# Optimization experiments

Measured on AMD Instinct MI355X. Metric: run time of the kernel, lower is better.

Reference implementation:

```python
import jax, jax.numpy as jnp
import numpy as np

BETA = 0.9
THR = 1.0
B, T, F, H = 64, 256, 1024, 512

# snntorch heaviside spike with ATan surrogate gradient (alpha=2.0, snntorch default)
@jax.custom_vjp
def spike_fn(u):
    return (u > 0).astype(u.dtype)

def _spike_fwd(u):
    return spike_fn(u), u

def _spike_bwd(u, g):
    alpha = 2.0
    grad = (alpha / 2.0) / (1.0 + (jnp.pi / 2.0 * alpha * u) ** 2)
    return (g * grad,)

spike_fn.defvjp(_spike_fwd, _spike_bwd)


def setup_inputs() -> dict:
    key = jax.random.key(0)
    ks = jax.random.split(key, 12)
    s = 0.05
    return {
        "f_f": jax.random.normal(ks[0], (B, T, F), dtype=jnp.float32),
        "seq_len": jnp.full((B,), T, dtype=jnp.int64),
        "Wf": jax.random.normal(ks[1], (H, F), dtype=jnp.float32) * s,
        "bf": jnp.zeros((H,), jnp.float32),
        "W1": jax.random.normal(ks[2], (H, H), dtype=jnp.float32) * s,
        "b1": jnp.zeros((H,), jnp.float32),
        "W2": jax.random.normal(ks[3], (H, H), dtype=jnp.float32) * s,
        "b2": jnp.zeros((H,), jnp.float32),
        "Mw1": jax.random.normal(ks[4], (512, H), dtype=jnp.float32) * s,
        "Mb1": jnp.zeros((512,), jnp.float32),
        "Mw2": jax.random.normal(ks[5], (32, 512), dtype=jnp.float32) * s,
        "Mb2": jnp.zeros((32,), jnp.float32),
        "Mw3": jax.random.normal(ks[6], (1, 32), dtype=jnp.float32) * s,
        "Mb3": jnp.zeros((1,), jnp.float32),
    }


def _forward(f_f, Wf, bf, W1, b1, W2, b2, Mw1, Mb1, Mw2, Mb2, Mw3, Mb3):
    h = f_f @ Wf.T + bf            # [B,T,H] fc_f
    x1 = h @ W1.T + b1             # layer-1 linear drive precomputed (state-independent)

    def step(carry, x1_t):
        m1, m2 = carry
        # snntorch Leaky (subtract reset): reset from previous mem's spike
        r1 = spike_fn(m1 - THR)
        m1 = BETA * m1 + x1_t - r1 * THR
        s1 = spike_fn(m1 - THR)
        x2 = s1 @ W2.T + b2        # layer-2 linear on spikes (dropout=identity, eval)
        r2 = spike_fn(m2 - THR)
        m2 = BETA * m2 + x2 - r2 * THR
        s2 = spike_fn(m2 - THR)
        return (m1, m2), s2

    init = (jnp.zeros((B, H), h.dtype), jnp.zeros((B, H), h.dtype))
    _, spk = jax.lax.scan(step, init, jnp.swapaxes(x1, 0, 1))  # [T,B,H]
    spk = jnp.swapaxes(spk, 0, 1)                              # [B,T,H]

    z = jax.nn.relu(spk @ Mw1.T + Mb1)
    z = z @ Mw2.T + Mb2
    logits = jax.nn.sigmoid((z @ Mw3.T + Mb3).squeeze(-1))     # [B,T]

    # filter: top-(seq_len//16 + 1) mean per clip; seq_len == T for all clips
    k = T // 16 + 1
    topv, _ = jax.lax.top_k(logits, k)
    return jnp.mean(topv, axis=-1)                             # [B]


def reference(f_f, seq_len, Wf, bf, W1, b1, W2, b2, Mw1, Mb1, Mw2, Mb2, Mw3, Mb3):
    return _forward(f_f, Wf, bf, W1, b1, W2, b2, Mw1, Mb1, Mw2, Mb2, Mw3, Mb3)
```

## Files before the change

### kernel.cpp

```cpp
#include <hip/hip_runtime.h>
#include <math.h>

#define BETA 0.9f
#define THR 1.0f

constexpr int B_ = 64, T_ = 256, F_ = 1024, H_ = 512;
constexpr int M_ = B_ * T_;

typedef float f32x4 __attribute__((ext_vector_type(4)));
typedef short short8 __attribute__((ext_vector_type(8)));
typedef _Float16 half8 __attribute__((ext_vector_type(8)));
typedef unsigned short us4 __attribute__((ext_vector_type(4)));
typedef unsigned short ushort_t;

static __device__ __forceinline__ unsigned short f2bf(float x) {
    unsigned b = __builtin_bit_cast(unsigned, x);
    unsigned r = (b + 0x7FFFu + ((b >> 16) & 1u)) >> 16;
    return (unsigned short)r;
}
static __device__ __forceinline__ float bf2f(unsigned short u) {
    unsigned v = ((unsigned)u) << 16;
    return __builtin_bit_cast(float, v);
}
static __device__ __forceinline__ unsigned short f2h(float x) {
    _Float16 h = (_Float16)x;
    return __builtin_bit_cast(unsigned short, h);
}
static __device__ __forceinline__ float h2f(unsigned short u) {
    return (float)__builtin_bit_cast(_Float16, u);
}
static __device__ __forceinline__ int swz(int r) {
    return ((r >> 2) & 3) ^ (r & 3);
}

#define GLDS(srcp, dstp)                                                      \
    __builtin_amdgcn_global_load_lds(                                         \
        (const __attribute__((address_space(1))) unsigned int*)(srcp),        \
        (__attribute__((address_space(3))) unsigned int*)(dstp), 16, 0, 0)

__global__ __launch_bounds__(256) void gemm_scan(
    const ushort_t* __restrict__ Ap, const ushort_t* __restrict__ Bp,
    const float* __restrict__ bias, ushort_t* __restrict__ Sout, int K) {
    __shared__ ushort_t lds[20480];

    const int tid = threadIdx.x;
    const int w = tid >> 6, l = tid & 63;
    const int flat = blockIdx.y * gridDim.x + blockIdx.x;
    const int clip = ((flat >> 6) << 3) | (flat & 7);
    const int strip = (flat >> 3) & 7;
    const int n0 = strip * 64;
    const int m0 = clip * 256;

    f32x4 acc[4][4];
#pragma unroll
    for (int mi = 0; mi < 4; ++mi)
#pragma unroll
        for (int ni = 0; ni < 4; ++ni) acc[mi][ni] = (f32x4){0.f, 0.f, 0.f, 0.f};

    const int c0 = l >> 4;
    const int schunk = (l & 7) ^ ((l >> 3) & 7);
    for (int k0 = 0; k0 < K; k0 += 64) {
        __syncthreads();
#pragma unroll
        for (int j = 0; j < 10; ++j) {
            const int seg = w * 10 + j;
            if (seg < 32) {
                const int r = seg * 8 + (l >> 3);
                GLDS(Ap + (size_t)(m0 + r) * K + k0 + schunk * 8,
                     &lds[seg * 512]);
            } else {
                const int r = (seg - 32) * 8 + (l >> 3);
                GLDS(Bp + (size_t)(n0 + r) * K + k0 + schunk * 8,
                     &lds[16384 + (seg - 32) * 512]);
            }
        }
        __syncthreads();

#pragma unroll
        for (int kh = 0; kh < 2; ++kh) {
            half8 aa[4], bb[4];
            const int q = kh * 4 + c0;
#pragma unroll
            for (int mi = 0; mi < 4; ++mi) {
                const int r = w * 64 + mi * 16 + (l & 15);
                const int off = r * 64 + ((q ^ (l & 7)) * 8);
                aa[mi] = __builtin_bit_cast(half8, *(const short8*)&lds[off]);
            }
#pragma unroll
            for (int ni = 0; ni < 4; ++ni) {
                const int r = ni * 16 + (l & 15);
                const int off = 16384 + r * 64 + ((q ^ (l & 7)) * 8);
                bb[ni] = __builtin_bit_cast(half8, *(const short8*)&lds[off]);
            }
#pragma unroll
            for (int mi = 0; mi < 4; ++mi)
#pragma unroll
                for (int ni = 0; ni < 4; ++ni)
                    acc[mi][ni] = __builtin_amdgcn_mfma_f32_16x16x32_f16(
                        aa[mi], bb[ni], acc[mi][ni], 0, 0, 0);
        }
    }

    __syncthreads();

    float bv[4];
#pragma unroll
    for (int ni = 0; ni < 4; ++ni) bv[ni] = bias[n0 + ni * 16 + (l & 15)];
#pragma unroll
    for (int mi = 0; mi < 4; ++mi) {
        const int t0 = w * 64 + mi * 16 + ((l >> 4) << 2);
#pragma unroll
        for (int ni = 0; ni < 4; ++ni) {
            const int h = ni * 16 + (l & 15);
#pragma unroll
            for (int r = 0; r < 4; ++r)
                lds[(t0 + r) * 66 + h] = f2h(acc[mi][ni][r] + bv[ni]);
        }
    }
    __syncthreads();

    if (tid < 64) {
        const int h = tid;
        ushort_t* sp = Sout + (size_t)m0 * 512 + n0 + h;
        float m = 0.f;
#pragma unroll 4
        for (int t = 0; t < T_; ++t) {
            const float xv = h2f(lds[t * 66 + h]);
            const float r = (m - THR > 0.f) ? THR : 0.f;
            m = BETA * m + xv - r;
            sp[(size_t)t * 512] = (m - THR > 0.f) ? (ushort_t)0x3C00 : (ushort_t)0;
        }
    }
}

__global__ __launch_bounds__(256) void gemm_mil(
    const ushort_t* __restrict__ Ap, const ushort_t* __restrict__ Bp,
    const float* __restrict__ bias, const float* __restrict__ Uv,
    float* __restrict__ part, int N, int K) {
    __shared__ ushort_t lds[16384];

    const int tid = threadIdx.x;
    const int w = tid >> 6, l = tid & 63;
    const int flat = blockIdx.y * gridDim.x + blockIdx.x;
    const int mt = ((flat >> 5) << 3) | (flat & 7);
    const int st = (flat >> 3) & 3;
    const int n0 = st * 128;
    const int m0 = mt * 128;
    const int wr = w >> 1, wc = w & 1;

    f32x4 acc[4][4];
#pragma unroll
    for (int mi = 0; mi < 4; ++mi)
#pragma unroll
        for (int ni = 0; ni < 4; ++ni) acc[mi][ni] = (f32x4){0.f, 0.f, 0.f, 0.f};

    const int c0 = l >> 4;
    const int schunk = (l & 7) ^ ((l >> 3) & 7);
    for (int k0 = 0; k0 < K; k0 += 64) {
        __syncthreads();
#pragma unroll
        for (int j = 0; j < 8; ++j) {
            const int g = w * 8 + j;
            const int seg = g & 15;
            const int r = seg * 8 + (l >> 3);
            const ushort_t* pl = (g < 16) ? Ap : Bp;
            const int rb = (g < 16) ? m0 : n0;
            GLDS(pl + (size_t)(rb + r) * K + k0 + schunk * 8, &lds[g * 512]);
        }
        __syncthreads();

#pragma unroll
        for (int kh = 0; kh < 2; ++kh) {
            half8 aa[4], bb[4];
            const int q = kh * 4 + c0;
#pragma unroll
            for (int mi = 0; mi < 4; ++mi) {
                const int r = wr * 64 + mi * 16 + (l & 15);
                const int off = r * 64 + ((q ^ (l & 7)) * 8);
                aa[mi] = __builtin_bit_cast(half8, *(const short8*)&lds[off]);
            }
#pragma unroll
            for (int ni = 0; ni < 4; ++ni) {
                const int r = wc * 64 + ni * 16 + (l & 15);
                const int off = 8192 + r * 64 + ((q ^ (l & 7)) * 8);
                bb[ni] = __builtin_bit_cast(half8, *(const short8*)&lds[off]);
            }
#pragma unroll
            for (int mi = 0; mi < 4; ++mi)
#pragma unroll
                for (int ni = 0; ni < 4; ++ni)
                    acc[mi][ni] = __builtin_amdgcn_mfma_f32_16x16x32_f16(
                        aa[mi], bb[ni], acc[mi][ni], 0, 0, 0);
        }
    }

    float bv[4], uc[4];
#pragma unroll
    for (int ni = 0; ni < 4; ++ni) {
        const int col = n0 + wc * 64 + ni * 16 + (l & 15);
        bv[ni] = bias[col];
        uc[ni] = Uv[col];
    }
    const int strip = (n0 >> 6) + wc;
#pragma unroll
    for (int mi = 0; mi < 4; ++mi) {
        float p[4];
#pragma unroll
        for (int r = 0; r < 4; ++r) {
            float s = 0.f;
#pragma unroll
            for (int ni = 0; ni < 4; ++ni)
                s += fmaxf(acc[mi][ni][r] + bv[ni], 0.f) * uc[ni];
            p[r] = s;
        }
#pragma unroll
        for (int off = 1; off <= 8; off <<= 1)
#pragma unroll
            for (int r = 0; r < 4; ++r) p[r] += __shfl_xor(p[r], off);
        if ((l & 15) == 0) {
            const int row0 = m0 + wr * 64 + mi * 16 + ((l >> 4) << 2);
#pragma unroll
            for (int r = 0; r < 4; ++r)
                part[(size_t)strip * M_ + row0 + r] = p[r];
        }
    }
}

__global__ __launch_bounds__(256) void gemm_bf16_wc(
    const ushort_t* __restrict__ Ah, const ushort_t* __restrict__ Al,
    const ushort_t* __restrict__ Bh, const ushort_t* __restrict__ Bl,
    ushort_t* __restrict__ Cout, int N, int K) {
    __shared__ ushort_t lds[4 * 4096];

    const int tid = threadIdx.x;
    const int w = tid >> 6, l = tid & 63;
    const int nwg = gridDim.x * gridDim.y;
    const int flat = blockIdx.y * gridDim.x + blockIdx.x;
    const int wg = (flat & 7) * (nwg >> 3) + (flat >> 3);
    const int n0 = (wg % gridDim.x) * 128;
    const int m0 = (wg / gridDim.x) * 128;
    const int wr = w >> 1, wc = w & 1;

    f32x4 acc[4][4];
#pragma unroll
    for (int mi = 0; mi < 4; ++mi)
#pragma unroll
        for (int ni = 0; ni < 4; ++ni) acc[mi][ni] = (f32x4){0.f, 0.f, 0.f, 0.f};

    const int c0 = l >> 4;
    for (int k0 = 0; k0 < K; k0 += 32) {
        __syncthreads();
#pragma unroll
        for (int j = 0; j < 8; ++j) {
            const int g = w * 8 + j;
            const int p = g >> 3, seg = g & 7;
            const int r = seg * 16 + (l >> 2);
            const int ch = (l & 3) ^ swz(r);
            const ushort_t* pl = (p == 0) ? Ah : (p == 1) ? Al : (p == 2) ? Bh : Bl;
            const int rb = (p < 2) ? m0 : n0;
            GLDS(pl + (size_t)(rb + r) * K + k0 + ch * 8,
                 &lds[p * 4096 + seg * 512]);
        }
        __syncthreads();

        short8 ah[4], al[4], bh[4], bl[4];
#pragma unroll
        for (int mi = 0; mi < 4; ++mi) {
            const int r = wr * 64 + mi * 16 + (l & 15);
            const int off = r * 32 + ((c0 ^ swz(r)) * 8);
            ah[mi] = *(const short8*)&lds[off];
            al[mi] = *(const short8*)&lds[4096 + off];
        }
#pragma unroll
        for (int ni = 0; ni < 4; ++ni) {
            const int r = wc * 64 + ni * 16 + (l & 15);
            const int off = r * 32 + ((c0 ^ swz(r)) * 8);
            bh[ni] = *(const short8*)&lds[8192 + off];
            bl[ni] = *(const short8*)&lds[12288 + off];
        }
#pragma unroll
        for (int mi = 0; mi < 4; ++mi)
#pragma unroll
            for (int ni = 0; ni < 4; ++ni) {
                acc[mi][ni] = __builtin_amdgcn_mfma_f32_16x16x32_bf16(
                    ah[mi], bh[ni], acc[mi][ni], 0, 0, 0);
                acc[mi][ni] = __builtin_amdgcn_mfma_f32_16x16x32_bf16(
                    ah[mi], bl[ni], acc[mi][ni], 0, 0, 0);
                acc[mi][ni] = __builtin_amdgcn_mfma_f32_16x16x32_bf16(
                    al[mi], bh[ni], acc[mi][ni], 0, 0, 0);
            }
    }

#pragma unroll
    for (int ni = 0; ni < 4; ++ni) {
        const int col = n0 + wc * 64 + ni * 16 + (l & 15);
#pragma unroll
        for (int mi = 0; mi < 4; ++mi) {
            const int row0 = m0 + wr * 64 + mi * 16 + ((l >> 4) << 2);
#pragma unroll
            for (int r = 0; r < 4; ++r)
                Cout[(size_t)(row0 + r) * N + col] = f2h(acc[mi][ni][r]);
        }
    }
}

__global__ __launch_bounds__(256) void prep_small(
    const float* __restrict__ W1, const float* __restrict__ W2,
    const float* __restrict__ Mw1, const float* __restrict__ bfv,
    const float* __restrict__ b1, const float* __restrict__ Mw2,
    const float* __restrict__ Mb2, const float* __restrict__ Mw3,
    const float* __restrict__ Mb3, const float* __restrict__ Wf,
    ushort_t* __restrict__ w1h, ushort_t* __restrict__ w1l,
    ushort_t* __restrict__ w2f, ushort_t* __restrict__ m1f,
    float* __restrict__ bc, float* __restrict__ uc,
    ushort_t* __restrict__ wfTh, ushort_t* __restrict__ wfTl) {
    __shared__ float tile[32][33];
    const int blk = blockIdx.x;
    const int tid = threadIdx.x;
    if (blk < 256) {
        const int i = blk * 256 + tid;
        f32x4 v = ((const f32x4*)W1)[i];
        us4 h, ll;
#pragma unroll
        for (int e = 0; e < 4; ++e) {
            const unsigned short hb = f2bf(v[e]);
            h[e] = hb;
            ll[e] = f2bf(v[e] - bf2f(hb));
        }
        ((us4*)w1h)[i] = h;
        ((us4*)w1l)[i] = ll;
    } else if (blk < 512) {
        const int i = (blk - 256) * 256 + tid;
        f32x4 v = ((const f32x4*)W2)[i];
        us4 h;
#pragma unroll
        for (int e = 0; e < 4; ++e) h[e] = f2h(v[e]);
        ((us4*)w2f)[i] = h;
    } else if (blk < 768) {
        const int i = (blk - 512) * 256 + tid;
        f32x4 v = ((const f32x4*)Mw1)[i];
        us4 h;
#pragma unroll
        for (int e = 0; e < 4; ++e) h[e] = f2h(v[e]);
        ((us4*)m1f)[i] = h;
    } else if (blk < 896) {
        const int w = tid >> 6, l = tid & 63;
        const int j = (blk - 768) * 4 + w;
        const float* row = W1 + (size_t)j * 512;
        float a = 0.f;
#pragma unroll
        for (int i = 0; i < 8; ++i) a += row[l + i * 64] * bfv[l + i * 64];
#pragma unroll
        for (int off = 32; off >= 1; off >>= 1) a += __shfl_xor(a, off);
        if (l == 0) bc[j] = a + b1[j];
    } else if (blk < 898) {
        const int j = (blk - 896) * 256 + tid;
        float a = 0.f;
        for (int i = 0; i < 32; ++i) a += Mw3[i] * Mw2[(size_t)i * 512 + j];
        uc[j] = a;
        if (j == 0) {
            float c = Mb3[0];
            for (int i = 0; i < 32; ++i) c += Mw3[i] * Mb2[i];
            uc[512] = c;
        }
    } else {
        const int idx = blk - 898;
        const int k0 = (idx & 31) * 32;
        const int i0 = (idx >> 5) * 32;
        const int tx = tid & 31;
        const int ty = tid >> 5;
#pragma unroll
        for (int e = 0; e < 4; ++e) {
            const int i = ty + e * 8;
            tile[i][tx] = Wf[(size_t)(i0 + i) * 1024 + k0 + tx];
        }
        __syncthreads();
#pragma unroll
        for (int e = 0; e < 4; ++e) {
            const int kk = ty + e * 8;
            const float v = tile[tx][kk];
            const unsigned short h = f2bf(v);
            wfTh[(size_t)(k0 + kk) * 512 + i0 + tx] = h;
            wfTl[(size_t)(k0 + kk) * 512 + i0 + tx] = f2bf(v - bf2f(h));
        }
    }
}

__global__ __launch_bounds__(256) void round_f16(const float* __restrict__ x,
                                                 ushort_t* __restrict__ o,
                                                 int n4) {
    int i = blockIdx.x * 256 + threadIdx.x;
    const int stride = gridDim.x * 256;
    for (; i < n4; i += stride) {
        f32x4 v = ((const f32x4*)x)[i];
        us4 h;
#pragma unroll
        for (int e = 0; e < 4; ++e) h[e] = f2h(v[e]);
        ((us4*)o)[i] = h;
    }
}

__global__ __launch_bounds__(64) void tail_topk(const float* __restrict__ part,
                                                const float* __restrict__ uc,
                                                float* __restrict__ out) {
    const int b = blockIdx.x;
    const int lane = threadIdx.x;
    const float c = uc[512];
    float v[4];
#pragma unroll
    for (int i = 0; i < 4; ++i) {
        const int row = b * T_ + lane + i * 64;
        float a = 0.f;
#pragma unroll
        for (int s = 0; s < 8; ++s) a += part[(size_t)s * M_ + row];
        v[i] = a + c;
    }
    float sum = 0.f;
    for (int iter = 0; iter < 17; ++iter) {
        float mv = v[0];
        int mslot = 0;
#pragma unroll
        for (int i = 1; i < 4; ++i)
            if (v[i] > mv) { mv = v[i]; mslot = i; }
        float bv = mv;
        int bl = lane, bs = mslot;
#pragma unroll
        for (int off = 32; off >= 1; off >>= 1) {
            const float ov = __shfl_xor(bv, off);
            const int ol = __shfl_xor(bl, off);
            const int os = __shfl_xor(bs, off);
            if (ov > bv || (ov == bv && ol < bl)) { bv = ov; bl = ol; bs = os; }
        }
        sum += 1.f / (1.f + expf(-bv));
        if (lane == bl) v[bs] = -1e30f;
    }
    if (lane == 0) out[b] = sum * (1.f / 17.f);
}

extern "C" void kernel_launch(void* const* d_in, const int* in_sizes, int n_in,
                              void* d_out, int out_size, void* d_ws, size_t ws_size,
                              hipStream_t stream) {
    const float* f_f = (const float*)d_in[0];
    const float* Wf  = (const float*)d_in[2];
    const float* bf  = (const float*)d_in[3];
    const float* W1  = (const float*)d_in[4];
    const float* b1  = (const float*)d_in[5];
    const float* W2  = (const float*)d_in[6];
    const float* b2  = (const float*)d_in[7];
    const float* Mw1 = (const float*)d_in[8];
    const float* Mb1 = (const float*)d_in[9];
    const float* Mw2 = (const float*)d_in[10];
    const float* Mb2 = (const float*)d_in[11];
    const float* Mw3 = (const float*)d_in[12];
    const float* Mb3 = (const float*)d_in[13];
    float* out = (float*)d_out;

    char* ws = (char*)d_ws;
    const size_t NEf = (size_t)M_ * F_;
    const size_t NE = (size_t)M_ * H_;
    ushort_t* ffh = (ushort_t*)ws;
    ushort_t* sbuf1 = ffh + NEf;
    ushort_t* sbuf2 = sbuf1 + NE;
    ushort_t* w1h = sbuf2 + NE;
    ushort_t* w1l = w1h + 262144;
    ushort_t* w2f = w1l + 262144;
    ushort_t* m1f = w2f + 262144;
    ushort_t* wfTh = m1f + 262144;
    ushort_t* wfTl = wfTh + 524288;
    ushort_t* wcf = wfTl + 524288;
    float* bc = (float*)(wcf + 524288);
    float* uc = bc + 512;
    float* part = uc + 513 + 63;

    const dim3 blk(256);

    prep_small<<<dim3(1410), blk, 0, stream>>>(W1, W2, Mw1, bf, b1, Mw2, Mb2,
                                               Mw3, Mb3, Wf, w1h, w1l, w2f,
                                               m1f, bc, uc, wfTh, wfTl);
    round_f16<<<dim3(2048), blk, 0, stream>>>(f_f, ffh, 4194304);

    gemm_bf16_wc<<<dim3(8, 4), blk, 0, stream>>>(w1h, w1l, wfTh, wfTl, wcf,
                                                 1024, 512);
    gemm_scan<<<dim3(8, 64), blk, 0, stream>>>(ffh, wcf, bc, sbuf1, 1024);
    gemm_scan<<<dim3(8, 64), blk, 0, stream>>>(sbuf1, w2f, b2, sbuf2, 512);
    gemm_mil<<<dim3(4, 128), blk, 0, stream>>>(sbuf2, m1f, Mb1, uc, part,
                                               512, 512);
    tail_topk<<<dim3(B_), dim3(64), 0, stream>>>(part, uc, out);
}
```

Baseline: 124.9 us.

## Double-buffer LDS in scan and MIL GEMMs; fold f16 rounding into prep kernel

The gemm_scan and gemm_mil kernels now keep two LDS buffers and issue the global-to-LDS loads for the next K tile before computing on the current one. This uses one barrier per iteration where there were two, and is meant to overlap memory latency with MFMA work. The standalone round_f16 launch is merged into prep_small as extra blocks, which saves one kernel launch. The cost is double the LDS per block (80KB for gemm_scan), which may lower occupancy. Correctness also relies on the single barrier per tile ordering the async load_lds writes against reads of the other buffer.

Measured after the change: 119.7 us. 1.04x faster.

```diff
diff --git a/kernel.cpp b/kernel.cpp
--- a/kernel.cpp
+++ b/kernel.cpp
@@ -41,7 +41,8 @@
 __global__ __launch_bounds__(256) void gemm_scan(
     const ushort_t* __restrict__ Ap, const ushort_t* __restrict__ Bp,
     const float* __restrict__ bias, ushort_t* __restrict__ Sout, int K) {
-    __shared__ ushort_t lds[20480];
+    constexpr int BUF = 20480;
+    __shared__ ushort_t lds[2 * BUF];
 
     const int tid = threadIdx.x;
     const int w = tid >> 6, l = tid & 63;
@@ -59,22 +60,30 @@
 
     const int c0 = l >> 4;
     const int schunk = (l & 7) ^ ((l >> 3) & 7);
-    for (int k0 = 0; k0 < K; k0 += 64) {
-        __syncthreads();
+
+    auto stage = [&](int buf, int k0) {
 #pragma unroll
         for (int j = 0; j < 10; ++j) {
             const int seg = w * 10 + j;
             if (seg < 32) {
                 const int r = seg * 8 + (l >> 3);
                 GLDS(Ap + (size_t)(m0 + r) * K + k0 + schunk * 8,
-                     &lds[seg * 512]);
+                     &lds[buf + seg * 512]);
             } else {
                 const int r = (seg - 32) * 8 + (l >> 3);
                 GLDS(Bp + (size_t)(n0 + r) * K + k0 + schunk * 8,
-                     &lds[16384 + (seg - 32) * 512]);
+                     &lds[buf + 16384 + (seg - 32) * 512]);
             }
         }
+    };
+
+    const int nt = K / 64;
+    stage(0, 0);
+    for (int t = 0; t < nt; ++t) {
+        const int cur = (t & 1) * BUF;
+        const int nxt = BUF - cur;
         __syncthreads();
+        if (t + 1 < nt) stage(nxt, (t + 1) * 64);
 
 #pragma unroll
         for (int kh = 0; kh < 2; ++kh) {
@@ -83,13 +92,13 @@
 #pragma unroll
             for (int mi = 0; mi < 4; ++mi) {
                 const int r = w * 64 + mi * 16 + (l & 15);
-                const int off = r * 64 + ((q ^ (l & 7)) * 8);
+                const int off = cur + r * 64 + ((q ^ (l & 7)) * 8);
                 aa[mi] = __builtin_bit_cast(half8, *(const short8*)&lds[off]);
             }
 #pragma unroll
             for (int ni = 0; ni < 4; ++ni) {
                 const int r = ni * 16 + (l & 15);
-                const int off = 16384 + r * 64 + ((q ^ (l & 7)) * 8);
+                const int off = cur + 16384 + r * 64 + ((q ^ (l & 7)) * 8);
                 bb[ni] = __builtin_bit_cast(half8, *(const short8*)&lds[off]);
             }
 #pragma unroll
@@ -100,8 +109,6 @@
                         aa[mi], bb[ni], acc[mi][ni], 0, 0, 0);
         }
     }
-
-    __syncthreads();
 
     float bv[4];
 #pragma unroll
@@ -137,7 +144,8 @@
     const ushort_t* __restrict__ Ap, const ushort_t* __restrict__ Bp,
     const float* __restrict__ bias, const float* __restrict__ Uv,
     float* __restrict__ part, int N, int K) {
-    __shared__ ushort_t lds[16384];
+    constexpr int BUF = 16384;
+    __shared__ ushort_t lds[2 * BUF];
 
     const int tid = threadIdx.x;
     const int w = tid >> 6, l = tid & 63;
@@ -156,8 +164,8 @@
 
     const int c0 = l >> 4;
     const int schunk = (l & 7) ^ ((l >> 3) & 7);
-    for (int k0 = 0; k0 < K; k0 += 64) {
-        __syncthreads();
+
+    auto stage = [&](int buf, int k0) {
 #pragma unroll
         for (int j = 0; j < 8; ++j) {
             const int g = w * 8 + j;
@@ -165,9 +173,18 @@
             const int r = seg * 8 + (l >> 3);
             const ushort_t* pl = (g < 16) ? Ap : Bp;
             const int rb = (g < 16) ? m0 : n0;
-            GLDS(pl + (size_t)(rb + r) * K + k0 + schunk * 8, &lds[g * 512]);
-        }
+            GLDS(pl + (size_t)(rb + r) * K + k0 + schunk * 8,
+                 &lds[buf + g * 512]);
+        }
+    };
+
+    const int nt = K / 64;
+    stage(0, 0);
+    for (int t = 0; t < nt; ++t) {
+        const int cur = (t & 1) * BUF;
+        const int nxt = BUF - cur;
         __syncthreads();
+        if (t + 1 < nt) stage(nxt, (t + 1) * 64);
 
 #pragma unroll
         for (int kh = 0; kh < 2; ++kh) {
@@ -176,13 +193,13 @@
 #pragma unroll
             for (int mi = 0; mi < 4; ++mi) {
                 const int r = wr * 64 + mi * 16 + (l & 15);
-                const int off = r * 64 + ((q ^ (l & 7)) * 8);
+                const int off = cur + r * 64 + ((q ^ (l & 7)) * 8);
                 aa[mi] = __builtin_bit_cast(half8, *(const short8*)&lds[off]);
             }
 #pragma unroll
             for (int ni = 0; ni < 4; ++ni) {
                 const int r = wc * 64 + ni * 16 + (l & 15);
-                const int off = 8192 + r * 64 + ((q ^ (l & 7)) * 8);
+                const int off = cur + 8192 + r * 64 + ((q ^ (l & 7)) * 8);
                 bb[ni] = __builtin_bit_cast(half8, *(const short8*)&lds[off]);
             }
 #pragma unroll
@@ -310,10 +327,11 @@
     const float* __restrict__ b1, const float* __restrict__ Mw2,
     const float* __restrict__ Mb2, const float* __restrict__ Mw3,
     const float* __restrict__ Mb3, const float* __restrict__ Wf,
-    ushort_t* __restrict__ w1h, ushort_t* __restrict__ w1l,
-    ushort_t* __restrict__ w2f, ushort_t* __restrict__ m1f,
-    float* __restrict__ bc, float* __restrict__ uc,
-    ushort_t* __restrict__ wfTh, ushort_t* __restrict__ wfTl) {
+    const float* __restrict__ f_f, ushort_t* __restrict__ w1h,
+    ushort_t* __restrict__ w1l, ushort_t* __restrict__ w2f,
+    ushort_t* __restrict__ m1f, float* __restrict__ bc,
+    float* __restrict__ uc, ushort_t* __restrict__ wfTh,
+    ushort_t* __restrict__ wfTl, ushort_t* __restrict__ ffh) {
     __shared__ float tile[32][33];
     const int blk = blockIdx.x;
     const int tid = threadIdx.x;
@@ -363,7 +381,7 @@
             for (int i = 0; i < 32; ++i) c += Mw3[i] * Mb2[i];
             uc[512] = c;
         }
-    } else {
+    } else if (blk < 1410) {
         const int idx = blk - 898;
         const int k0 = (idx & 31) * 32;
         const int i0 = (idx >> 5) * 32;
@@ -383,20 +401,16 @@
             wfTh[(size_t)(k0 + kk) * 512 + i0 + tx] = h;
             wfTl[(size_t)(k0 + kk) * 512 + i0 + tx] = f2bf(v - bf2f(h));
         }
-    }
-}
-
-__global__ __launch_bounds__(256) void round_f16(const float* __restrict__ x,
-                                                 ushort_t* __restrict__ o,
-                                                 int n4) {
-    int i = blockIdx.x * 256 + threadIdx.x;
-    const int stride = gridDim.x * 256;
-    for (; i < n4; i += stride) {
-        f32x4 v = ((const f32x4*)x)[i];
-        us4 h;
-#pragma unroll
-        for (int e = 0; e < 4; ++e) h[e] = f2h(v[e]);
-        ((us4*)o)[i] = h;
+    } else {
+        constexpr int n4 = 4194304;
+        const int base = (blk - 1410) * 256 + tid;
+        for (int i = base; i < n4; i += 2048 * 256) {
+            f32x4 v = ((const f32x4*)f_f)[i];
+            us4 h;
+#pragma unroll
+            for (int e = 0; e < 4; ++e) h[e] = f2h(v[e]);
+            ((us4*)ffh)[i] = h;
+        }
     }
 }
 
@@ -474,10 +488,10 @@
 
     const dim3 blk(256);
 
-    prep_small<<<dim3(1410), blk, 0, stream>>>(W1, W2, Mw1, bf, b1, Mw2, Mb2,
-                                               Mw3, Mb3, Wf, w1h, w1l, w2f,
-                                               m1f, bc, uc, wfTh, wfTl);
-    round_f16<<<dim3(2048), blk, 0, stream>>>(f_f, ffh, 4194304);
+    prep_small<<<dim3(3458), blk, 0, stream>>>(W1, W2, Mw1, bf, b1, Mw2, Mb2,
+                                               Mw3, Mb3, Wf, f_f, w1h, w1l,
+                                               w2f, m1f, bc, uc, wfTh, wfTl,
+                                               ffh);
 
     gemm_bf16_wc<<<dim3(8, 4), blk, 0, stream>>>(w1h, w1l, wfTh, wfTl, wcf,
                                                  1024, 512);
```
